# Kernel optimization log

Measured on AMD Instinct MI355X. Metric: run time of the kernel, lower is better.

Reference implementation:

```python
import jax, jax.numpy as jnp
import numpy as np

T, B, D = 1024, 8, 1024
H, DH, FF = 16, 64, 4096
BG = 0.1  # GRU gating bias constant
SCALE = 1.0 / DH ** 0.5


def layer_norm(x, g, b, eps=1e-5):
    mu = jnp.mean(x, axis=-1, keepdims=True)
    var = jnp.var(x, axis=-1, keepdims=True)
    return (x - mu) * jax.lax.rsqrt(var + eps) * g + b


def gru_gate(x, y, W, U, bz):
    # W, U: [3, D, D] stacking (r, z, g) projections; bz: Uz bias
    r = jax.nn.sigmoid(y @ W[0] + x @ U[0])
    z = jax.nn.sigmoid(y @ W[1] + x @ U[1] + bz - BG)
    h = jnp.tanh(y @ W[2] + r * (x @ U[2]))
    return (1.0 - z) * x + z * h


def setup_inputs() -> dict:
    key = jax.random.key(0)
    ks = jax.random.split(key, 16)
    s = 0.02
    inp = {
        "x": jax.random.normal(ks[0], (T, B, D), jnp.float32),
        "Wq": jax.random.normal(ks[1], (D, H * DH), jnp.float32) * s,
        "Wk": jax.random.normal(ks[2], (D, H * DH), jnp.float32) * s,
        "Wv": jax.random.normal(ks[3], (D, H * DH), jnp.float32) * s,
        "Wo": jax.random.normal(ks[4], (H * DH, D), jnp.float32) * s,
        "ln1_g": jnp.ones((D,), jnp.float32),
        "ln1_b": jnp.zeros((D,), jnp.float32),
        "W1": jax.random.normal(ks[5], (D, FF), jnp.float32) * s,
        "b1": jnp.zeros((FF,), jnp.float32),
        "W2": jax.random.normal(ks[6], (FF, D), jnp.float32) * s,
        "b2": jnp.zeros((D,), jnp.float32),
        "ln2_g": jnp.ones((D,), jnp.float32),
        "ln2_b": jnp.zeros((D,), jnp.float32),
        "gate1_W": jax.random.normal(ks[7], (3, D, D), jnp.float32) * s,
        "gate1_U": jax.random.normal(ks[8], (3, D, D), jnp.float32) * s,
        "gate1_bz": jnp.zeros((D,), jnp.float32),
        "gate2_W": jax.random.normal(ks[9], (3, D, D), jnp.float32) * s,
        "gate2_U": jax.random.normal(ks[10], (3, D, D), jnp.float32) * s,
        "gate2_bz": jnp.zeros((D,), jnp.float32),
        "attn_mask": jnp.triu(jnp.ones((T, T), bool), k=1),  # causal: mask j > i
    }
    return inp


def reference(x, Wq, Wk, Wv, Wo, ln1_g, ln1_b, W1, b1, W2, b2,
              ln2_g, ln2_b, gate1_W, gate1_U, gate1_bz,
              gate2_W, gate2_U, gate2_bz, attn_mask):
    # --- multihead attention (pre_lnorm=True) ---
    xn = layer_norm(x, ln1_g, ln1_b)                     # [T,B,D]
    q = (xn @ Wq).reshape(T, B, H, DH)
    k = (xn @ Wk).reshape(T, B, H, DH)
    v = (xn @ Wv).reshape(T, B, H, DH)
    scores = jnp.einsum('ibhd,jbhd->ijbh', q, k) * SCALE  # [T,T,B,H]
    scores = jnp.where(attn_mask[:, :, None, None], -jnp.inf, scores)
    probs = jax.nn.softmax(scores, axis=1)
    attn = jnp.einsum('ijbh,jbhd->ibhd', probs, v).reshape(T, B, H * DH)
    src2 = attn @ Wo                                      # [T,B,D]
    # --- GRU gate 1 ---
    src = gru_gate(x, src2, gate1_W, gate1_U, gate1_bz)
    # --- positionwise FFN (pre_lnorm=True) ---
    sn = layer_norm(src, ln2_g, ln2_b)
    ff = jax.nn.relu(sn @ W1 + b1) @ W2 + b2
    # --- GRU gate 2 ---
    return gru_gate(src, ff, gate2_W, gate2_U, gate2_bz)
```

## Files before the change

kernel.cpp:

```cpp
#include <hip/hip_runtime.h>
#include <hip/hip_bf16.h>

#define T_  1024
#define B_  8
#define D_  1024
#define H_  16
#define DH_ 64
#define FF_ 4096
#define MROWS (T_*B_)

typedef __attribute__((ext_vector_type(8))) short short8;
typedef __attribute__((ext_vector_type(4))) float f32x4;
typedef __attribute__((ext_vector_type(4))) unsigned short us4;
typedef __attribute__((ext_vector_type(4))) unsigned int  u32x4;

__device__ __forceinline__ unsigned short f2b(float f){
  unsigned int u = __builtin_bit_cast(unsigned int, f);
  u += 0x7FFFu + ((u >> 16) & 1u);
  return (unsigned short)(u >> 16);
}
__device__ __forceinline__ float b2f(unsigned short h){
  unsigned int u = ((unsigned int)h) << 16;
  return __builtin_bit_cast(float, u);
}

__device__ __forceinline__ void glds16(const unsigned short* g, unsigned short* l){
  __builtin_amdgcn_global_load_lds(
    (const __attribute__((address_space(1))) unsigned int*)g,
    (__attribute__((address_space(3))) unsigned int*)l, 16, 0, 0);
}

enum { FRELU=1 };

template<int BN>
__global__ __launch_bounds__(512, 2) void gemm256(
    const unsigned short* __restrict__ A1, const unsigned short* __restrict__ A2,
    int K1, long lda,
    const unsigned short* __restrict__ Bt, long ldb,
    unsigned short* __restrict__ C, long ldc,
    const float* __restrict__ bias, int K, int flags,
    const unsigned short* __restrict__ A1b, const unsigned short* __restrict__ Btb,
    int N1)
{
  constexpr int BM = 256, BK = 32;
  constexpr int NBQ = BN/128;
  constexpr int S   = 2 + NBQ;
  constexpr int WN  = BN/64;
  constexpr int BUFSZ = 16384 + BN*64;
  extern __shared__ char L[];

  int t = threadIdx.x, w = t >> 6, l = t & 63;

  int nx = gridDim.x;
  int nwg = nx * gridDim.y;
  int lin = blockIdx.y*nx + blockIdx.x;
  if (!(nwg & 7)) lin = (lin & 7)*(nwg >> 3) + (lin >> 3);
  int bx = lin % nx, by = lin / nx;
  int m0 = by*BM, n0 = bx*BN;

  const unsigned short* Aa = A1;
  const unsigned short* Ab = A2;
  const unsigned short* Bb = Bt;
  if (n0 >= N1){ Aa = A1b; Ab = A1b; Bb = Btb - (long)N1*ldb; }

  int srow[2], sce[2];
  #pragma unroll
  for (int q=0;q<2;q++){
    int p  = q*8192 + w*1024 + l*16;
    int sp = p ^ (((p>>7)&3)<<4);
    srow[q] = sp >> 6;
    sce[q]  = (sp & 63) >> 1;
  }

  auto stage = [&](int buf, int kt){
    int k0 = kt*BK;
    const unsigned short* ap; int ko;
    if (k0 < K1){ ap = Aa; ko = k0; } else { ap = Ab; ko = k0 - K1; }
    char* ab = L + buf*BUFSZ;
    char* bb = ab + 16384;
    #pragma unroll
    for (int q=0;q<2;q++)
      glds16(ap + (long)(m0 + srow[q])*lda + ko + sce[q],
             (unsigned short*)(ab + q*8192 + w*1024));
    #pragma unroll
    for (int q=0;q<NBQ;q++)
      glds16(Bb + (long)(n0 + srow[q])*ldb + k0 + sce[q],
             (unsigned short*)(bb + q*8192 + w*1024));
  };

  f32x4 acc[8][WN];
  #pragma unroll
  for (int m=0;m<8;m++)
    #pragma unroll
    for (int n=0;n<WN;n++) acc[m][n] = (f32x4){0.f,0.f,0.f,0.f};

  int wr = w >> 2, wc = w & 3;
  int fr = l & 15, fq = l >> 4;
  int nk = K / BK;

  stage(0, 0);
  stage(1, 1);
  stage(2, 2);
  if constexpr (S == 4) asm volatile("s_waitcnt vmcnt(8)" ::: "memory");
  else                  asm volatile("s_waitcnt vmcnt(6)" ::: "memory");
  __builtin_amdgcn_s_barrier();
  asm volatile("" ::: "memory");

  int cur = 0;
  for (int kt = 0; kt < nk; ++kt){
    if (kt + 3 < nk) stage((cur + 3) & 3, kt + 3);

    const char* ab = L + cur*BUFSZ;
    const char* bb = ab + 16384;
    short8 af[8], bf[WN];
    #pragma unroll
    for (int n=0;n<WN;n++){
      int r = wc*(BN/4) + n*16 + fr;
      bf[n] = *(const short8*)(bb + ((r*64 + fq*16) ^ (((r>>1)&3)<<4)));
    }
    #pragma unroll
    for (int m=0;m<8;m++){
      int r = wr*128 + m*16 + fr;
      af[m] = *(const short8*)(ab + ((r*64 + fq*16) ^ (((r>>1)&3)<<4)));
    }
    __builtin_amdgcn_s_setprio(1);
    #pragma unroll
    for (int m=0;m<8;m++)
      #pragma unroll
      for (int n=0;n<WN;n++)
        acc[m][n] = __builtin_amdgcn_mfma_f32_16x16x32_bf16(af[m], bf[n], acc[m][n], 0,0,0);
    __builtin_amdgcn_s_setprio(0);

    int c = nk - 1 - kt; if (c > 3) c = 3;
    if (c == 3){
      if constexpr (S == 4) asm volatile("s_waitcnt vmcnt(8)" ::: "memory");
      else                  asm volatile("s_waitcnt vmcnt(6)" ::: "memory");
    } else if (c == 2){
      if constexpr (S == 4) asm volatile("s_waitcnt vmcnt(4)" ::: "memory");
      else                  asm volatile("s_waitcnt vmcnt(3)" ::: "memory");
    } else if (c == 1){
      asm volatile("s_waitcnt vmcnt(0)" ::: "memory");
    }
    if (c > 0){
      __builtin_amdgcn_s_barrier();
      asm volatile("" ::: "memory");
    }
    cur = (cur + 1) & 3;
  }

  int r0 = m0 + wr*128 + (fq << 2);
  int c0 = n0 + wc*(BN/4) + fr;
  #pragma unroll
  for (int m=0;m<8;m++)
    #pragma unroll
    for (int n=0;n<WN;n++){
      int col = c0 + n*16;
      float bv = bias ? bias[col] : 0.f;
      #pragma unroll
      for (int j=0;j<4;j++){
        float v = acc[m][n][j] + bv;
        if (flags & FRELU) v = v > 0.f ? v : 0.f;
        C[(long)(r0 + m*16 + j)*ldc + col] = f2b(v);
      }
    }
}

__global__ __launch_bounds__(256) void flash_attn(
  const unsigned short* __restrict__ qkv, const unsigned short* __restrict__ vT,
  unsigned short* __restrict__ O)
{
  int p = blockIdx.x, z = blockIdx.y;
  int b = z >> 4, h = z & 15;
  const unsigned short* Vz = vT + (long)z*DH_*T_;

  __shared__ unsigned short Ks[64*64];
  __shared__ unsigned short Vs[64*64];
  __shared__ unsigned short Ps[4][32][72];

  int t = threadIdx.x, w = t >> 6, l = t & 63;
  int fr = l & 15, fg = l >> 4;
  int srow = t >> 2, sc = (t & 3) * 16;

  for (int rep = 0; rep < 2; ++rep){
    int qt = rep ? (7 - p) : p;
    int q0 = qt*128 + w*32;

    short8 qf[2][2];
    #pragma unroll
    for (int m=0;m<2;m++)
      #pragma unroll
      for (int ks=0;ks<2;ks++)
        qf[m][ks] = *(const short8*)(qkv + ((long)(q0 + m*16 + fr)*B_ + b)*3072 + h*DH_ + ks*32 + fg*8);

    f32x4 oacc[2][4];
    float mr[2][4], lr[2][4];
    #pragma unroll
    for (int m=0;m<2;m++){
      #pragma unroll
      for (int n=0;n<4;n++) oacc[m][n] = (f32x4){0.f,0.f,0.f,0.f};
      #pragma unroll
      for (int j=0;j<4;j++){ mr[m][j] = -1e30f; lr[m][j] = 0.f; }
    }

    int nkv = (qt + 1) * 2;
    for (int kt = 0; kt < nkv; ++kt){
      int kv0 = kt * 64;
      __syncthreads();
      {
        const unsigned short* kg = qkv + ((long)(kv0+srow)*B_ + b)*3072 + 1024 + h*DH_ + sc;
        const unsigned short* vg = Vz + (long)srow*T_ + kv0 + sc;
        int rb = srow*128, sw = (srow & 7) << 4;
        *(u32x4*)((char*)Ks + ((rb + sc*2     ) ^ sw)) = *(const u32x4*)(kg);
        *(u32x4*)((char*)Ks + ((rb + sc*2 + 16) ^ sw)) = *(const u32x4*)(kg + 8);
        *(u32x4*)((char*)Vs + ((rb + sc*2     ) ^ sw)) = *(const u32x4*)(vg);
        *(u32x4*)((char*)Vs + ((rb + sc*2 + 16) ^ sw)) = *(const u32x4*)(vg + 8);
      }
      __syncthreads();

      if (kv0 <= q0 + 31){
        f32x4 sacc[2][4];
        #pragma unroll
        for (int m=0;m<2;m++)
          #pragma unroll
          for (int n=0;n<4;n++) sacc[m][n] = (f32x4){0.f,0.f,0.f,0.f};
        __builtin_amdgcn_s_setprio(1);
        #pragma unroll
        for (int ks=0;ks<2;ks++){
          short8 kf[4];
          #pragma unroll
          for (int n=0;n<4;n++){
            int r = n*16 + fr;
            kf[n] = *(const short8*)((const char*)Ks + ((r*128 + ks*64 + fg*16) ^ ((r & 7) << 4)));
          }
          #pragma unroll
          for (int m=0;m<2;m++)
            #pragma unroll
            for (int n=0;n<4;n++)
              sacc[m][n] = __builtin_amdgcn_mfma_f32_16x16x32_bf16(qf[m][ks], kf[n], sacc[m][n], 0,0,0);
        }
        __builtin_amdgcn_s_setprio(0);

        #pragma unroll
        for (int m=0;m<2;m++)
          #pragma unroll
          for (int j=0;j<4;j++){
            int qg = q0 + m*16 + fg*4 + j;
            float vmax = -1e30f;
            #pragma unroll
            for (int n=0;n<4;n++){
              int kg = kv0 + n*16 + fr;
              float s = (kg <= qg) ? sacc[m][n][j]*0.125f : -1e30f;
              sacc[m][n][j] = s;
              vmax = fmaxf(vmax, s);
            }
            #pragma unroll
            for (int msk=1; msk<16; msk<<=1) vmax = fmaxf(vmax, __shfl_xor(vmax, msk));
            float mnew = fmaxf(mr[m][j], vmax);
            float sc_o = __expf(mr[m][j] - mnew);
            mr[m][j] = mnew;
            float rsum = 0.f;
            #pragma unroll
            for (int n=0;n<4;n++){
              float pv = __expf(sacc[m][n][j] - mnew);
              sacc[m][n][j] = pv;
              rsum += pv;
            }
            #pragma unroll
            for (int msk=1; msk<16; msk<<=1) rsum += __shfl_xor(rsum, msk);
            lr[m][j] = lr[m][j]*sc_o + rsum;
            #pragma unroll
            for (int n=0;n<4;n++) oacc[m][n][j] *= sc_o;
          }

        #pragma unroll
        for (int m=0;m<2;m++)
          #pragma unroll
          for (int n=0;n<4;n++)
            #pragma unroll
            for (int j=0;j<4;j++)
              Ps[w][m*16 + fg*4 + j][n*16 + fr] = f2b(sacc[m][n][j]);

        __builtin_amdgcn_s_setprio(1);
        #pragma unroll
        for (int ks=0;ks<2;ks++){
          short8 pf[2], vf[4];
          #pragma unroll
          for (int m=0;m<2;m++) pf[m] = *(const short8*)&Ps[w][m*16+fr][ks*32+fg*8];
          #pragma unroll
          for (int n=0;n<4;n++){
            int r = n*16 + fr;
            vf[n] = *(const short8*)((const char*)Vs + ((r*128 + ks*64 + fg*16) ^ ((r & 7) << 4)));
          }
          #pragma unroll
          for (int m=0;m<2;m++)
            #pragma unroll
            for (int n=0;n<4;n++)
              oacc[m][n] = __builtin_amdgcn_mfma_f32_16x16x32_bf16(pf[m], vf[n], oacc[m][n], 0,0,0);
        }
        __builtin_amdgcn_s_setprio(0);
      }
    }

    #pragma unroll
    for (int m=0;m<2;m++)
      #pragma unroll
      for (int j=0;j<4;j++){
        float inv = 1.f / lr[m][j];
        long i = q0 + m*16 + fg*4 + j;
        #pragma unroll
        for (int n=0;n<4;n++)
          O[(i*B_ + b)*(long)D_ + h*DH_ + n*16 + fr] = f2b(oacc[m][n][j] * inv);
      }
  }
}

__global__ __launch_bounds__(256) void ln_cast(const float* __restrict__ X,
    const float* __restrict__ g, const float* __restrict__ bta,
    unsigned short* __restrict__ xn, unsigned short* __restrict__ xbf)
{
  long row = blockIdx.x;
  int t = threadIdx.x;
  f32x4 xv = ((const f32x4*)(X + row*D_))[t];
  float s = xv[0]+xv[1]+xv[2]+xv[3];
  float q = xv[0]*xv[0]+xv[1]*xv[1]+xv[2]*xv[2]+xv[3]*xv[3];
  #pragma unroll
  for (int o=32;o;o>>=1){ s += __shfl_xor(s,o); q += __shfl_xor(q,o); }
  __shared__ float rs[4], rq[4];
  int w = t >> 6;
  if ((t & 63) == 0){ rs[w]=s; rq[w]=q; }
  __syncthreads();
  s = rs[0]+rs[1]+rs[2]+rs[3];
  q = rq[0]+rq[1]+rq[2]+rq[3];
  float mean = s * (1.f/D_);
  float var  = q * (1.f/D_) - mean*mean;
  float rstd = rsqrtf(var + 1e-5f);
  f32x4 gv = ((const f32x4*)g)[t];
  f32x4 bv = ((const f32x4*)bta)[t];
  us4 o, raw;
  #pragma unroll
  for (int jj=0;jj<4;jj++){
    o[jj]   = f2b((xv[jj]-mean)*rstd*gv[jj] + bv[jj]);
    raw[jj] = f2b(xv[jj]);
  }
  ((us4*)(xn  + row*D_))[t] = o;
  ((us4*)(xbf + row*D_))[t] = raw;
}

__global__ __launch_bounds__(256) void tr_f2b(const float* __restrict__ src,
    unsigned short* __restrict__ dst, int N, long ldd)
{
  __shared__ float tile[32][33];
  int k0 = blockIdx.x*32, n0 = blockIdx.y*32;
  int tx = threadIdx.x & 31, ty = threadIdx.x >> 5;
  #pragma unroll
  for (int i=0;i<4;i++)
    tile[ty+i*8][tx] = src[(long)(k0+ty+i*8)*N + n0 + tx];
  __syncthreads();
  #pragma unroll
  for (int i=0;i<4;i++)
    dst[(long)(n0+ty+i*8)*ldd + k0 + tx] = f2b(tile[tx][ty+i*8]);
}

__global__ __launch_bounds__(256) void tr_gate(const float* __restrict__ gW,
    const float* __restrict__ gU, unsigned short* __restrict__ Wb)
{
  __shared__ float tile[32][33];
  int z = blockIdx.z;
  int c = z >> 1;
  const float* src = ((z & 1) ? gU : gW) + (size_t)c*1048576;
  unsigned short* dst; long ldd;
  if (c < 2){ dst = Wb + (size_t)c*(1024*2048) + (z&1)*1024; ldd = 2048; }
  else      { dst = Wb + (size_t)(4 + (z&1))*1048576;        ldd = 1024; }
  int k0 = blockIdx.x*32, n0 = blockIdx.y*32;
  int tx = threadIdx.x & 31, ty = threadIdx.x >> 5;
  #pragma unroll
  for (int i=0;i<4;i++)
    tile[ty+i*8][tx] = src[(long)(k0+ty+i*8)*1024 + n0 + tx];
  __syncthreads();
  #pragma unroll
  for (int i=0;i<4;i++)
    dst[(long)(n0+ty+i*8)*ldd + k0 + tx] = f2b(tile[tx][ty+i*8]);
}

__global__ __launch_bounds__(256) void build_vT(const unsigned short* __restrict__ vsrc,
                                                unsigned short* __restrict__ vT)
{
  __shared__ unsigned short tile[32][33];
  int z = blockIdx.z, b = z >> 4, h = z & 15;
  int t0 = blockIdx.x*32, d0 = blockIdx.y*32;
  int tx = threadIdx.x & 31, ty = threadIdx.x >> 5;
  #pragma unroll
  for (int i=0;i<4;i++)
    tile[ty+i*8][tx] = vsrc[((long)(t0+ty+i*8)*B_ + b)*3072 + h*DH_ + d0 + tx];
  __syncthreads();
  #pragma unroll
  for (int i=0;i<4;i++)
    vT[(long)z*DH_*T_ + (long)(d0+ty+i*8)*T_ + t0 + tx] = tile[tx][ty+i*8];
}

__global__ __launch_bounds__(256) void gru_combine(
  const unsigned short* __restrict__ rz,
  const unsigned short* __restrict__ yx,
  const float* __restrict__ xin, const float* __restrict__ bz,
  float* __restrict__ of, unsigned short* __restrict__ ob,
  const float* __restrict__ lng, const float* __restrict__ lnb,
  unsigned short* __restrict__ sn)
{
  int t = threadIdx.x;
  long row = blockIdx.x;
  long i = row*1024 + t*4;
  int col = t*4;
  us4 r4 = *(const us4*)(rz + row*2048 + col);
  us4 z4 = *(const us4*)(rz + row*2048 + 1024 + col);
  us4 a4 = *(const us4*)(yx + row*2048 + col);
  us4 b4 = *(const us4*)(yx + row*2048 + 1024 + col);
  f32x4 xv = *(const f32x4*)(xin + i);
  f32x4 bzv = *(const f32x4*)(bz + col);
  f32x4 o;
  #pragma unroll
  for (int jj=0;jj<4;jj++){
    float r = 1.f/(1.f + __expf(-b2f(r4[jj])));
    float z = 1.f/(1.f + __expf(-(b2f(z4[jj]) + bzv[jj] - 0.1f)));
    float h = tanhf(b2f(a4[jj]) + r*b2f(b4[jj]));
    o[jj] = (1.f - z)*xv[jj] + z*h;
  }
  *(f32x4*)(of+i) = o;
  if (ob){
    us4 q;
    #pragma unroll
    for (int jj=0;jj<4;jj++) q[jj] = f2b(o[jj]);
    *(us4*)(ob+i) = q;
  }
  if (sn){
    float s = o[0]+o[1]+o[2]+o[3];
    float q = o[0]*o[0]+o[1]*o[1]+o[2]*o[2]+o[3]*o[3];
    #pragma unroll
    for (int off=32;off;off>>=1){ s += __shfl_xor(s,off); q += __shfl_xor(q,off); }
    __shared__ float rs[4], rq[4];
    int w = t >> 6;
    if ((t & 63) == 0){ rs[w]=s; rq[w]=q; }
    __syncthreads();
    s = rs[0]+rs[1]+rs[2]+rs[3];
    q = rq[0]+rq[1]+rq[2]+rq[3];
    float mean = s * (1.f/D_);
    float var  = q * (1.f/D_) - mean*mean;
    float rstd = rsqrtf(var + 1e-5f);
    f32x4 gv = ((const f32x4*)lng)[t];
    f32x4 bv = ((const f32x4*)lnb)[t];
    us4 oq;
    #pragma unroll
    for (int jj=0;jj<4;jj++) oq[jj] = f2b((o[jj]-mean)*rstd*gv[jj] + bv[jj]);
    *(us4*)(sn+i) = oq;
  }
}

extern "C" void kernel_launch(void* const* d_in, const int* in_sizes, int n_in,
                              void* d_out, int out_size, void* d_ws, size_t ws_size,
                              hipStream_t stream)
{
  const float* x    = (const float*)d_in[0];
  const float* Wq   = (const float*)d_in[1];
  const float* Wk   = (const float*)d_in[2];
  const float* Wv   = (const float*)d_in[3];
  const float* Wo   = (const float*)d_in[4];
  const float* ln1g = (const float*)d_in[5];
  const float* ln1b = (const float*)d_in[6];
  const float* W1   = (const float*)d_in[7];
  const float* b1   = (const float*)d_in[8];
  const float* W2   = (const float*)d_in[9];
  const float* b2   = (const float*)d_in[10];
  const float* ln2g = (const float*)d_in[11];
  const float* ln2b = (const float*)d_in[12];
  const float* g1W  = (const float*)d_in[13];
  const float* g1U  = (const float*)d_in[14];
  const float* g1bz = (const float*)d_in[15];
  const float* g2W  = (const float*)d_in[16];
  const float* g2U  = (const float*)d_in[17];
  const float* g2bz = (const float*)d_in[18];
  float* out = (float*)d_out;

  const size_t MB = 1u << 20;
  if (ws_size < 144*MB) return;
  char* base = (char*)d_ws;

  (void)hipFuncSetAttribute((const void*)gemm256<256>,
                            hipFuncAttributeMaxDynamicSharedMemorySize, 131072);
  (void)hipFuncSetAttribute((const void*)gemm256<128>,
                            hipFuncAttributeMaxDynamicSharedMemorySize, 98304);

  unsigned short* W    = (unsigned short*)(base);
  unsigned short* x_bf = (unsigned short*)(base + 16*MB);
  unsigned short* sbf  = (unsigned short*)(base + 32*MB);
  unsigned short* src2 = (unsigned short*)(base + 48*MB);
  unsigned short* qkv  = (unsigned short*)(base + 64*MB);
  unsigned short* vT   = (unsigned short*)(base + 112*MB);
  unsigned short* attn = (unsigned short*)(base + 128*MB);
  unsigned short* xn   = attn;
  unsigned short* rz   = (unsigned short*)(base + 64*MB);
  unsigned short* yx   = (unsigned short*)(base + 96*MB);
  unsigned short* sn   = x_bf;
  unsigned short* ff1  = (unsigned short*)(base + 80*MB);
  unsigned short* ffb  = src2;

  const size_t E1M = 1048576;
  unsigned short* BtRZ = W;
  unsigned short* W2g  = W + 4*E1M;
  unsigned short* U2g  = W + 5*E1M;
  unsigned short* W1T  = W;
  unsigned short* W2T  = W + 4*E1M;
  unsigned short* Wqkv = W;
  unsigned short* WoT  = W + 3*E1M;

  const int NOSPLIT = 1 << 30;
  dim3 blk(256);
  auto G2 = [&](const unsigned short* A1, const unsigned short* A2, int K1, long lda,
                const unsigned short* Bt, long ldb, unsigned short* C, long ldc,
                const float* bias, int M, int N, int K, int flags,
                const unsigned short* A1b, const unsigned short* Btb, int N1){
    gemm256<256><<<dim3(N/256, M/256), dim3(512), 131072, stream>>>(
        A1,A2,K1,lda,Bt,ldb,C,ldc,bias,K,flags,A1b,Btb,N1);
  };
  auto G2n = [&](const unsigned short* A1, const unsigned short* A2, int K1, long lda,
                 const unsigned short* Bt, long ldb, unsigned short* C, long ldc,
                 const float* bias, int M, int N, int K, int flags){
    gemm256<128><<<dim3(N/128, M/256), dim3(512), 98304, stream>>>(
        A1,A2,K1,lda,Bt,ldb,C,ldc,bias,K,flags,A1,Bt,NOSPLIT);
  };

  tr_f2b<<<dim3(32,32), blk, 0, stream>>>(Wq, Wqkv,          D_, D_);
  tr_f2b<<<dim3(32,32), blk, 0, stream>>>(Wk, Wqkv + 1*E1M,  D_, D_);
  tr_f2b<<<dim3(32,32), blk, 0, stream>>>(Wv, Wqkv + 2*E1M,  D_, D_);
  tr_f2b<<<dim3(32,32), blk, 0, stream>>>(Wo, WoT,           D_, D_);
  ln_cast<<<dim3(MROWS), blk, 0, stream>>>(x, ln1g, ln1b, xn, x_bf);

  G2(xn, xn, D_, D_, Wqkv, D_, qkv, 3072, nullptr, MROWS, 3072, D_, 0, xn, Wqkv, NOSPLIT);
  build_vT<<<dim3(32,2,128), blk, 0, stream>>>(qkv + 2048, vT);
  flash_attn<<<dim3(4, B_*H_), blk, 0, stream>>>(qkv, vT, attn);
  G2n(attn, attn, D_, D_, WoT, D_, src2, D_, nullptr, MROWS, D_, D_, 0);

  tr_gate<<<dim3(32,32,6), blk, 0, stream>>>(g1W, g1U, W);
  G2(src2, x_bf, D_, D_, BtRZ, 2048, rz, 2048, nullptr, MROWS, 2048, 2048, 0, src2, BtRZ, NOSPLIT);
  G2(src2, src2, D_, D_, W2g, D_, yx, 2048, nullptr, MROWS, 2048, D_, 0, x_bf, U2g, 1024);
  gru_combine<<<dim3(MROWS), blk, 0, stream>>>(rz, yx, x, g1bz, out, sbf, ln2g, ln2b, sn);

  tr_f2b<<<dim3(32,128), blk, 0, stream>>>(W1, W1T, FF_, D_);
  tr_f2b<<<dim3(128,32), blk, 0, stream>>>(W2, W2T, D_, FF_);
  G2(sn, sn, D_, D_, W1T, D_, ff1, FF_, b1, MROWS, FF_, D_, FRELU, sn, W1T, NOSPLIT);
  G2n(ff1, ff1, FF_, FF_, W2T, FF_, ffb, D_, b2, MROWS, D_, FF_, 0);

  tr_gate<<<dim3(32,32,6), blk, 0, stream>>>(g2W, g2U, W);
  G2(ffb, sbf, D_, D_, BtRZ, 2048, rz, 2048, nullptr, MROWS, 2048, 2048, 0, ffb, BtRZ, NOSPLIT);
  G2(ffb, ffb, D_, D_, W2g, D_, yx, 2048, nullptr, MROWS, 2048, D_, 0, sbf, U2g, 1024);
  gru_combine<<<dim3(MROWS), blk, 0, stream>>>(rz, yx, out, g2bz, out, nullptr, nullptr, nullptr, nullptr);
}
```

Baseline: 697.8 us.

## Split GEMM main loop into two phases interleaving prefetch with MFMA

For the BN=256 GEMM variant, each k-iteration now runs in two halves. The A-tile prefetch is issued after the first half of the fragment loads and the B-tile prefetch after the second, with barriers and sched_barriers around each half's MFMA block. The aim is to interleave global-to-LDS traffic with matrix math, in the style of ping-pong scheduling, and to lower register pressure by loading only half the A fragments at a time. It adds two extra barriers per iteration, and the vmcnt accounting has to stay valid with split staging.

```diff
diff --git a/kernel.cpp b/kernel.cpp
--- a/kernel.cpp
+++ b/kernel.cpp
@@ -72,16 +72,19 @@
     sce[q]  = (sp & 63) >> 1;
   }
 
-  auto stage = [&](int buf, int kt){
+  auto stageA = [&](int buf, int kt){
     int k0 = kt*BK;
     const unsigned short* ap; int ko;
     if (k0 < K1){ ap = Aa; ko = k0; } else { ap = Ab; ko = k0 - K1; }
     char* ab = L + buf*BUFSZ;
-    char* bb = ab + 16384;
     #pragma unroll
     for (int q=0;q<2;q++)
       glds16(ap + (long)(m0 + srow[q])*lda + ko + sce[q],
              (unsigned short*)(ab + q*8192 + w*1024));
+  };
+  auto stageB = [&](int buf, int kt){
+    int k0 = kt*BK;
+    char* bb = L + buf*BUFSZ + 16384;
     #pragma unroll
     for (int q=0;q<NBQ;q++)
       glds16(Bb + (long)(n0 + srow[q])*ldb + k0 + sce[q],
@@ -98,9 +101,9 @@
   int fr = l & 15, fq = l >> 4;
   int nk = K / BK;
 
-  stage(0, 0);
-  stage(1, 1);
-  stage(2, 2);
+  stageA(0, 0); stageB(0, 0);
+  stageA(1, 1); stageB(1, 1);
+  stageA(2, 2); stageB(2, 2);
   if constexpr (S == 4) asm volatile("s_waitcnt vmcnt(8)" ::: "memory");
   else                  asm volatile("s_waitcnt vmcnt(6)" ::: "memory");
   __builtin_amdgcn_s_barrier();
@@ -108,28 +111,74 @@
 
   int cur = 0;
   for (int kt = 0; kt < nk; ++kt){
-    if (kt + 3 < nk) stage((cur + 3) & 3, kt + 3);
-
     const char* ab = L + cur*BUFSZ;
     const char* bb = ab + 16384;
-    short8 af[8], bf[WN];
-    #pragma unroll
-    for (int n=0;n<WN;n++){
-      int r = wc*(BN/4) + n*16 + fr;
-      bf[n] = *(const short8*)(bb + ((r*64 + fq*16) ^ (((r>>1)&3)<<4)));
+    bool pf = (kt + 3 < nk);
+    int pbuf = (cur + 3) & 3;
+
+    if constexpr (BN == 256){
+      short8 af0[4], af1[4], bf[WN];
+      #pragma unroll
+      for (int n=0;n<WN;n++){
+        int r = wc*(BN/4) + n*16 + fr;
+        bf[n] = *(const short8*)(bb + ((r*64 + fq*16) ^ (((r>>1)&3)<<4)));
+      }
+      #pragma unroll
+      for (int m=0;m<4;m++){
+        int r = wr*128 + m*16 + fr;
+        af0[m] = *(const short8*)(ab + ((r*64 + fq*16) ^ (((r>>1)&3)<<4)));
+      }
+      if (pf) stageA(pbuf, kt + 3);
+      __builtin_amdgcn_s_barrier();
+      asm volatile("s_waitcnt lgkmcnt(0)" ::: "memory");
+      __builtin_amdgcn_sched_barrier(0);
+      __builtin_amdgcn_s_setprio(1);
+      #pragma unroll
+      for (int m=0;m<4;m++)
+        #pragma unroll
+        for (int n=0;n<WN;n++)
+          acc[m][n] = __builtin_amdgcn_mfma_f32_16x16x32_bf16(af0[m], bf[n], acc[m][n], 0,0,0);
+      __builtin_amdgcn_s_setprio(0);
+      __builtin_amdgcn_s_barrier();
+      asm volatile("" ::: "memory");
+
+      #pragma unroll
+      for (int m=0;m<4;m++){
+        int r = wr*128 + (m+4)*16 + fr;
+        af1[m] = *(const short8*)(ab + ((r*64 + fq*16) ^ (((r>>1)&3)<<4)));
+      }
+      if (pf) stageB(pbuf, kt + 3);
+      __builtin_amdgcn_s_barrier();
+      asm volatile("s_waitcnt lgkmcnt(0)" ::: "memory");
+      __builtin_amdgcn_sched_barrier(0);
+      __builtin_amdgcn_s_setprio(1);
+      #pragma unroll
+      for (int m=0;m<4;m++)
+        #pragma unroll
+        for (int n=0;n<WN;n++)
+          acc[m+4][n] = __builtin_amdgcn_mfma_f32_16x16x32_bf16(af1[m], bf[n], acc[m+4][n], 0,0,0);
+      __builtin_amdgcn_s_setprio(0);
+    } else {
+      if (pf){ stageA(pbuf, kt + 3); stageB(pbuf, kt + 3); }
+      short8 af[8], bf[WN];
+      #pragma unroll
+      for (int n=0;n<WN;n++){
+        int r = wc*(BN/4) + n*16 + fr;
+        bf[n] = *(const short8*)(bb + ((r*64 + fq*16) ^ (((r>>1)&3)<<4)));
+      }
+      #pragma unroll
+      for (int m=0;m<8;m++){
+        int r = wr*128 + m*16 + fr;
+        af[m] = *(const short8*)(ab + ((r*64 + fq*16) ^ (((r>>1)&3)<<4)));
+      }
+      __builtin_amdgcn_s_setprio(1);
+      #pragma unroll
+      for (int m=0;m<8;m++)
+        #pragma unroll
+        for (int n=0;n<WN;n++)
+          acc[m][n] = __builtin_amdgcn_mfma_f32_16x16x32_bf16(af[m], bf[n], acc[m][n], 0,0,0);
+      __builtin_amdgcn_s_setprio(0);
     }
-    #pragma unroll
-    for (int m=0;m<8;m++){
-      int r = wr*128 + m*16 + fr;
-      af[m] = *(const short8*)(ab + ((r*64 + fq*16) ^ (((r>>1)&3)<<4)));
-    }
-    __builtin_amdgcn_s_setprio(1);
-    #pragma unroll
-    for (int m=0;m<8;m++)
-      #pragma unroll
-      for (int n=0;n<WN;n++)
-        acc[m][n] = __builtin_amdgcn_mfma_f32_16x16x32_bf16(af[m], bf[n], acc[m][n], 0,0,0);
-    __builtin_amdgcn_s_setprio(0);
 
     int c = nk - 1 - kt; if (c > 3) c = 3;
     if (c == 3){
```

New measurement: 706.8 us. Within noise of the previous version (+1.3%).
